# Kernel tuning notes

Measured on AMD Instinct MI355X. Metric: run time of the kernel, lower is better.

The kernel has to match this reference:

```python
import jax, jax.numpy as jnp
import numpy as np


def _refl_conv(x, w, b, pad, stride):
    # ReflectionPad2d(pad) followed by Conv2d(stride=stride), NCHW / OIHW layouts.
    x = jnp.pad(x, ((0, 0), (0, 0), (pad, pad), (pad, pad)), mode='reflect')
    y = jax.lax.conv_general_dilated(
        x, w, window_strides=(stride, stride), padding='VALID',
        dimension_numbers=('NCHW', 'OIHW', 'NCHW'))
    return y + b[None, :, None, None]


def setup_inputs() -> dict:
    key = jax.random.key(0)
    ks = jax.random.split(key, 16)
    B, C, H, W = 8, 128, 64, 64
    IH, IW = 4 * H, 4 * W
    g = 0.02  # init gain ('normal' init in source)
    f32 = jnp.float32
    return {
        'feature_in': jax.random.normal(ks[0], (B, C, H, W), f32),
        'imgs': jax.random.uniform(ks[1], (B, 3, IH, IW), dtype=f32),
        'masks': jax.random.uniform(ks[2], (B, 1, IH, IW), dtype=f32),
        # Gate conv stack params (torch OIHW layout), biases zero per init_weights
        'gw1': g * jax.random.normal(ks[3], (32, 4, 7, 7), f32),
        'gb1': jnp.zeros((32,), f32),
        'gw2': g * jax.random.normal(ks[4], (64, 32, 5, 5), f32),
        'gb2': jnp.zeros((64,), f32),
        'gw3': g * jax.random.normal(ks[5], (128, 64, 5, 5), f32),
        'gb3': jnp.zeros((128,), f32),
        'gw4': g * jax.random.normal(ks[6], (256, 128, 3, 3), f32),
        'gb4': jnp.zeros((256,), f32),
        'gw5': g * jax.random.normal(ks[7], (1, 256, 3, 3), f32),
        'gb5': jnp.zeros((1,), f32),
        # combiner: Conv2d(2C -> C, 1x1)
        'cw': g * jax.random.normal(ks[8], (C, 2 * C, 1, 1), f32),
        'cb': jnp.zeros((C,), f32),
    }


def reference(feature_in, imgs, masks, gw1, gb1, gw2, gb2, gw3, gb3,
              gw4, gb4, gw5, gb5, cw, cb):
    PI = 3.1415926
    # ---- Gate ----
    x = jnp.concatenate([imgs, masks], axis=1)          # [B,4,4H,4W]
    s = jax.nn.relu(_refl_conv(x, gw1, gb1, 3, 1))
    s = jax.nn.relu(_refl_conv(s, gw2, gb2, 2, 2))
    s = jax.nn.relu(_refl_conv(s, gw3, gb3, 2, 1))
    s = jax.nn.relu(_refl_conv(s, gw4, gb4, 1, 2))
    s = jax.nn.relu(_refl_conv(s, gw5, gb5, 1, 1))      # [B,1,H,W]
    s = jnp.tan(PI * (jnp.tanh(s) - 0.5))
    B, C, H, W = feature_in.shape
    P = H * W
    gate = s.reshape(B, P, 1, 1)                        # row-major pixel order
    # ---- Att (patch_size=1: kernels are per-pixel feature vectors) ----
    K = feature_in.reshape(B, C, P).transpose(0, 2, 1) + 1e-7   # [B,P,C]
    Kn = K / jnp.sqrt(jnp.sum(K * K, axis=-1, keepdims=True))
    # attention_scores = conv2d(feature_map, K_norm) == cosine-like similarity
    scores = jnp.einsum('bpc,bcyx->bpyx', Kn, feature_in) + gate  # [B,P,H,W]
    A = jax.nn.softmax(scores, axis=1)
    # conv_transpose2d with 1x1 kernels == weighted sum of (unnormalized) kernels
    att = jnp.einsum('bpyx,bpc->bcyx', A, K)            # [B,C,H,W]
    # ---- combiner (1x1 conv on concat) ----
    cat = jnp.concatenate([att, feature_in], axis=1)    # [B,2C,H,W]
    out = jnp.einsum('oc,bcyx->boyx', cw[:, :, 0, 0], cat) + cb[None, :, None, None]
    return out
```

## Files before the change

### kernel.cpp

```cpp
#include <hip/hip_runtime.h>
#include <hip/hip_bf16.h>
#include <hip/hip_fp16.h>
#include <math.h>


#define PI_F 3.1415926f

typedef __attribute__((ext_vector_type(8))) short short8;
typedef __attribute__((ext_vector_type(4))) float f32x4;
typedef _Float16 half8 __attribute__((ext_vector_type(8)));
typedef __attribute__((ext_vector_type(4))) unsigned short u16x4;
typedef unsigned short ushort_t;

__device__ __forceinline__ ushort_t f2bf(float x) {
    unsigned u = __float_as_uint(x);
    unsigned r = (u + 0x7FFFu + ((u >> 16) & 1u)) >> 16;
    return (ushort_t)r;
}
__device__ __forceinline__ void split16(float x, ushort_t& h, ushort_t& l) {
    __half hh = __float2half(x);
    h = __half_as_ushort(hh);
    l = __half_as_ushort(__float2half(x - __half2float(hh)));
}
__device__ __forceinline__ ushort_t f2h(float x) {
    return __half_as_ushort(__float2half(x));
}
__device__ __forceinline__ int swz(int r, int c) {
    return ((c ^ r ^ (r >> 2)) & 3) << 3;
}

__global__ __launch_bounds__(256) void transform_w_k(
    const float* __restrict__ w, ushort_t* __restrict__ Wh, ushort_t* __restrict__ Wl,
    int Cout, int Cin, int KK)
{
    int idx = blockIdx.x * 256 + threadIdx.x;
    int N = Cout * Cin * KK;
    if (idx >= N) return;
    int oc = idx / (Cin * KK);
    int rem = idx - oc * (Cin * KK);
    int ic = rem / KK;
    int t = rem - ic * KK;
    float v = w[idx];
    long dst = ((long)t * Cout + oc) * Cin + ic;
    split16(v, Wh[dst], Wl[dst]);
}

__global__ __launch_bounds__(256) void transform_w1_k(
    const float* __restrict__ w, ushort_t* __restrict__ Wh, ushort_t* __restrict__ Wl)
{
    int idx = blockIdx.x * 256 + threadIdx.x;
    if (idx >= 7 * 32 * 32) return;
    int ky = idx / 1024;
    int rem = idx - ky * 1024;
    int oc = rem >> 5;
    int k = rem & 31;
    float v = 0.f;
    if (k < 28) {
        int kx = k >> 2, ic = k & 3;
        v = w[((oc * 4 + ic) * 7 + ky) * 7 + kx];
    }
    split16(v, Wh[idx], Wl[idx]);
}

__global__ __launch_bounds__(256) void prep_in_k(
    const float* __restrict__ imgs, const float* __restrict__ masks,
    ushort_t* __restrict__ Xh)
{
    const int iy = blockIdx.x, b = blockIdx.y;
    int sy = iy - 3; if (sy < 0) sy = -sy; if (sy >= 256) sy = 510 - sy;
    const int rb = sy << 8;
    const float* i0 = imgs + (long)b * 3 * 65536;
    const float* mk = masks + (long)b * 65536;
    for (int x = threadIdx.x; x < 262; x += 256) {
        int sx = x - 3; if (sx < 0) sx = -sx; if (sx >= 256) sx = 510 - sx;
        u16x4 hv;
        hv[0] = f2h(i0[rb + sx]);
        hv[1] = f2h(i0[65536 + rb + sx]);
        hv[2] = f2h(i0[131072 + rb + sx]);
        hv[3] = f2h(mk[rb + sx]);
        long o = ((long)(b * 262 + iy) * 262 + x) * 4;
        *(u16x4*)&Xh[o] = hv;
    }
}

__global__ __launch_bounds__(256) void conv1_mfma_k(
    const ushort_t* __restrict__ Xinh,
    const ushort_t* __restrict__ W1h, const ushort_t* __restrict__ W1l,
    const float* __restrict__ bias, ushort_t* __restrict__ Oh)
{
    const int tid = threadIdx.x, lane = tid & 63, wid = tid >> 6;
    const int wm = wid & 1, wn = wid >> 1, l15 = lane & 15, quad = lane >> 4;
    const int ox0 = blockIdx.x * 64;
    const int oy = blockIdx.y, b = blockIdx.z;
    f32x4 acc[2];
    acc[0] = (f32x4){0.f, 0.f, 0.f, 0.f};
    acc[1] = (f32x4){0.f, 0.f, 0.f, 0.f};
#pragma unroll
    for (int ky = 0; ky < 7; ++ky) {
        long wo = (long)(ky * 32 + wm * 16 + l15) * 32 + quad * 8;
        half8 Ah = *(const half8*)&W1h[wo];
        half8 Al = *(const half8*)&W1l[wo];
        long xrow = ((long)(b * 262 + oy + ky) * 262 + ox0) * 4;
#pragma unroll
        for (int ni = 0; ni < 2; ++ni) {
            long xo = xrow + (wn * 32 + ni * 16 + l15) * 4 + quad * 8;
            half8 Bh = *(const half8*)&Xinh[xo];
            acc[ni] = __builtin_amdgcn_mfma_f32_16x16x32_f16(Ah, Bh, acc[ni], 0, 0, 0);
            acc[ni] = __builtin_amdgcn_mfma_f32_16x16x32_f16(Al, Bh, acc[ni], 0, 0, 0);
        }
    }
    const int ocf = wm * 16 + quad * 4;
    float4 bv = *(const float4*)&bias[ocf];
#pragma unroll
    for (int ni = 0; ni < 2; ++ni) {
        int n = ox0 + wn * 32 + ni * 16 + l15;
        u16x4 hv;
        hv[0] = f2h(fmaxf(acc[ni][0] + bv.x, 0.f));
        hv[1] = f2h(fmaxf(acc[ni][1] + bv.y, 0.f));
        hv[2] = f2h(fmaxf(acc[ni][2] + bv.z, 0.f));
        hv[3] = f2h(fmaxf(acc[ni][3] + bv.w, 0.f));
        long o = ((long)(b * 260 + oy + 2) * 260 + n + 2) * 32 + ocf;
        *(u16x4*)&Oh[o] = hv;
    }
}

__global__ __launch_bounds__(256) void pad_cl_k(
    ushort_t* __restrict__ Xh, int Hp, int Wp, int PAD, int C, int H, int W)
{
    const int iy = blockIdx.x, b = blockIdx.y;
    int t = iy - PAD; if (t < 0) t = -t; if (t >= H) t = 2 * H - 2 - t;
    const int iys = t + PAD;
    const long rowd = ((long)(b * Hp + iy) * Wp) * C;
    const long rows = ((long)(b * Hp + iys) * Wp) * C;
    const int nch = Wp * (C >> 3);
    for (int idx = threadIdx.x; idx < nch; idx += 256) {
        int x = idx / (C >> 3);
        int cg = (idx - x * (C >> 3)) << 3;
        int t2 = x - PAD; if (t2 < 0) t2 = -t2; if (t2 >= W) t2 = 2 * W - 2 - t2;
        int xs = t2 + PAD;
        if (xs == x && iys == iy) continue;
        *(int4*)&Xh[rowd + (long)x * C + cg] = *(const int4*)&Xh[rows + (long)xs * C + cg];
    }
}

template<int K, int S, int CIN, int CSTG, int MT, int NPX, bool WRITE_CL>
__global__ __launch_bounds__(256, 2) void conv_mfma_k(
    const ushort_t* __restrict__ Xh,
    const ushort_t* __restrict__ Wh, const ushort_t* __restrict__ Wl,
    const float* __restrict__ bias,
    int Hp, int Wp, int CoutT,
    ushort_t* __restrict__ Oh, int Hpn, int Wpn, int NP,
    float* __restrict__ Ofp)
{
    constexpr int WS = (NPX - 1) * S + K;
    constexpr int WS2 = (WS + 1) / 2;
    constexpr int MF = MT / 32;
    constexpr int NF = NPX / 32;
    __shared__ ushort_t Bsh[WS * CSTG];
    __shared__ ushort_t Ash[K * MT * CSTG];
    __shared__ ushort_t Asl[K * MT * CSTG];
    const int tid = threadIdx.x, lane = tid & 63, wid = tid >> 6;
    const int wm = wid & 1, wn = wid >> 1, l15 = lane & 15, quad = lane >> 4;
    const int bx = blockIdx.x, oy = blockIdx.y;
    const int NOC = CoutT / MT;
    const int ocg = blockIdx.z % NOC, b = blockIdx.z / NOC;
    const int ox0 = bx * NPX;

    f32x4 acc[MF][NF];
#pragma unroll
    for (int mi = 0; mi < MF; ++mi)
#pragma unroll
        for (int ni = 0; ni < NF; ++ni) acc[mi][ni] = (f32x4){0.f, 0.f, 0.f, 0.f};

#pragma unroll
    for (int ky = 0; ky < K; ++ky) {
        const long rowoff = ((long)(b * Hp + oy * S + ky) * Wp + ox0 * S) * CIN;
        for (int cs = 0; cs < CIN; cs += CSTG) {
            __syncthreads();
            constexpr int NCH = WS * CSTG / 8;
#pragma unroll
            for (int it = 0; it < (NCH + 255) / 256; ++it) {
                int flat = tid + it * 256;
                if (flat < NCH) {
                    int e0 = flat * 8;
                    int x = e0 / CSTG;
                    int cpos = (e0 - x * CSTG) >> 3;
                    int xs = (S == 1) ? x : ((x >> 1) + (x & 1) * WS2);
                    *(int4*)&Bsh[xs * CSTG + swz(xs, cpos)] =
                        *(const int4*)&Xh[rowoff + (long)x * CIN + cs + cpos * 8];
                }
            }
            constexpr int NW = K * MT * CSTG / 8;
#pragma unroll
            for (int it = 0; it < (NW + 255) / 256; ++it) {
                int flat = tid + it * 256;
                if (flat < NW) {
                    int e0 = flat * 8;
                    int kx = e0 / (MT * CSTG);
                    int rem = e0 - kx * MT * CSTG;
                    int oc = rem / CSTG;
                    int cpos = (rem - oc * CSTG) >> 3;
                    int arow = kx * MT + oc;
                    int dst = arow * CSTG + swz(arow, cpos);
                    long src = ((long)((ky * K + kx) * CoutT + ocg * MT + oc)) * CIN + cs + cpos * 8;
                    *(int4*)&Ash[dst] = *(const int4*)&Wh[src];
                    *(int4*)&Asl[dst] = *(const int4*)&Wl[src];
                }
            }
            __syncthreads();
#pragma unroll
            for (int kx = 0; kx < K; ++kx) {
                half8 Ah[MF], Al[MF], Bh[NF];
#pragma unroll
                for (int mi = 0; mi < MF; ++mi) {
                    int arow = kx * MT + wm * (MT / 2) + mi * 16 + l15;
                    int ao = arow * CSTG + swz(arow, quad);
                    Ah[mi] = *(const half8*)&Ash[ao];
                    Al[mi] = *(const half8*)&Asl[ao];
                }
#pragma unroll
                for (int ni = 0; ni < NF; ++ni) {
                    int m = wn * (NPX / 2) + ni * 16 + l15;
                    int xs = (S == 1) ? (m + kx) : (m + (kx >> 1) + (kx & 1) * WS2);
                    Bh[ni] = *(const half8*)&Bsh[xs * CSTG + swz(xs, quad)];
                }
#pragma unroll
                for (int mi = 0; mi < MF; ++mi)
#pragma unroll
                    for (int ni = 0; ni < NF; ++ni) {
                        acc[mi][ni] = __builtin_amdgcn_mfma_f32_16x16x32_f16(Ah[mi], Bh[ni], acc[mi][ni], 0, 0, 0);
                        acc[mi][ni] = __builtin_amdgcn_mfma_f32_16x16x32_f16(Al[mi], Bh[ni], acc[mi][ni], 0, 0, 0);
                    }
            }
        }
    }
#pragma unroll
    for (int ni = 0; ni < NF; ++ni) {
        const int n = ox0 + wn * (NPX / 2) + ni * 16 + l15;
#pragma unroll
        for (int mi = 0; mi < MF; ++mi) {
            const int ocf = ocg * MT + wm * (MT / 2) + mi * 16 + quad * 4;
            float4 bv = *(const float4*)&bias[ocf];
            float v0 = fmaxf(acc[mi][ni][0] + bv.x, 0.f);
            float v1 = fmaxf(acc[mi][ni][1] + bv.y, 0.f);
            float v2 = fmaxf(acc[mi][ni][2] + bv.z, 0.f);
            float v3 = fmaxf(acc[mi][ni][3] + bv.w, 0.f);
            if (WRITE_CL) {
                long o = ((long)(b * Hpn + oy + NP) * Wpn + n + NP) * CoutT + ocf;
                u16x4 hv;
                hv[0] = f2h(v0); hv[1] = f2h(v1); hv[2] = f2h(v2); hv[3] = f2h(v3);
                *(u16x4*)&Oh[o] = hv;
            } else {
                long o = ((long)(b * CoutT + ocf) << 12) + (oy << 6) + n;
                Ofp[o] = v0;
                Ofp[o + 4096] = v1;
                Ofp[o + 8192] = v2;
                Ofp[o + 12288] = v3;
            }
        }
    }
}

__global__ __launch_bounds__(256) void conv5_gate_k(
    const float* __restrict__ s4, const float* __restrict__ w,
    const float* __restrict__ bias, float* __restrict__ gate)
{
    const int tid = threadIdx.x;
    const int lane = tid & 63, g = tid >> 6;
    const int oy = blockIdx.x, b = blockIdx.y;
    int ixo[3], iyo[3];
#pragma unroll
    for (int k = 0; k < 3; ++k) {
        int ix = lane + k - 1; if (ix < 0) ix = -ix; if (ix >= 64) ix = 126 - ix;
        int iy = oy + k - 1; if (iy < 0) iy = -iy; if (iy >= 64) iy = 126 - iy;
        ixo[k] = ix; iyo[k] = iy << 6;
    }
    float part = 0.f;
    const float* inb = s4 + ((long)b * 256 + g * 64) * 4096;
    const float* wg = w + g * 64 * 9;
    for (int ic = 0; ic < 64; ++ic) {
        const float* inc = inb + ic * 4096;
        const float* wc = wg + ic * 9;
#pragma unroll
        for (int ky = 0; ky < 3; ++ky)
#pragma unroll
            for (int kx = 0; kx < 3; ++kx)
                part = fmaf(wc[ky * 3 + kx], inc[iyo[ky] + ixo[kx]], part);
    }
    __shared__ float red[4][64];
    red[g][lane] = part;
    __syncthreads();
    if (tid < 64) {
        float s = bias[0] + red[0][tid] + red[1][tid] + red[2][tid] + red[3][tid];
        s = fmaxf(s, 0.f);
        gate[(b << 12) + (oy << 6) + tid] = tanf(PI_F * (tanhf(s) - 0.5f));
    }
}

__global__ __launch_bounds__(256) void invn_k(const float* __restrict__ F, float* __restrict__ invn)
{
    const int p = blockIdx.x * 256 + threadIdx.x;
    const int b = blockIdx.y;
    const float* Fb = F + (long)b * 524288;
    float ss = 0.f;
#pragma unroll 8
    for (int c = 0; c < 128; ++c) {
        float v = Fb[c * 4096 + p] + 1e-7f;
        ss = fmaf(v, v, ss);
    }
    invn[(b << 12) + p] = 1.0f / sqrtf(ss);
}

__global__ __launch_bounds__(256) void prep_bf16_k(
    const float* __restrict__ F, ushort_t* __restrict__ Fo16, ushort_t* __restrict__ Ft16)
{
    __shared__ float Ls[128][65];
    const int tid = threadIdx.x;
    const int lane = tid & 63, wv = tid >> 6;
    const int p0 = blockIdx.x * 64, b = blockIdx.y;
#pragma unroll 8
    for (int cc = 0; cc < 32; ++cc) {
        int c = wv * 32 + cc;
        long idx = ((long)b * 128 + c) * 4096 + p0 + lane;
        float v = F[idx];
        Fo16[idx] = f2bf(v);
        Ls[c][lane] = v;
    }
    __syncthreads();
#pragma unroll 8
    for (int i = 0; i < 32; ++i) {
        int flat = tid + 256 * i;
        int c = flat & 127, pl_ = flat >> 7;
        Ft16[((long)b * 4096 + p0 + pl_) * 128 + c] = f2bf(Ls[c][pl_]);
    }
}

__global__ __launch_bounds__(256, 4) void flash_attn_k(
    const ushort_t* __restrict__ Ft16, const ushort_t* __restrict__ Fo16,
    const float* __restrict__ invn, const float* __restrict__ gate,
    float* __restrict__ Opart, float* __restrict__ lpart)
{
    __shared__ float redS[64][4];
    __shared__ ushort_t Es[2][64][72];
    __shared__ ushort_t Qs[16 * 64 * 8];
    const int tid = threadIdx.x, lane = tid & 63, w = tid >> 6;
    const int l15 = lane & 15, quad = lane >> 4;
    const int q0 = blockIdx.x * 64;
    const int ks = blockIdx.y, b = blockIdx.z;
    const int bp = b << 12;
    const ushort_t* Ftb = Ft16 + (long)b * 4096 * 128;
    const ushort_t* Fob = Fo16 + (long)b * 128 * 4096;

#pragma unroll
    for (int s = tid; s < 1024; s += 256) {
        int f = s >> 6, ls = s & 63;
        int ni = f >> 2, cs = f & 3;
        int q = q0 + ni * 16 + (ls & 15);
        int c = cs * 32 + (ls >> 4) * 8;
        *(short8*)&Qs[s * 8] = *(const short8*)&Ftb[(long)q * 128 + c];
    }

    f32x4 O[2][4];
#pragma unroll
    for (int mi = 0; mi < 2; ++mi)
#pragma unroll
        for (int ni = 0; ni < 4; ++ni) O[mi][ni] = (f32x4){0.f, 0.f, 0.f, 0.f};
    float l_acc[4] = {0.f, 0.f, 0.f, 0.f};

    __syncthreads();

    const int p_beg = ks * 1024;
    int buf = 0;
    for (int p0 = p_beg; p0 < p_beg + 1024; p0 += 64, buf ^= 1) {
        f32x4 Sa[4];
#pragma unroll
        for (int ni = 0; ni < 4; ++ni) Sa[ni] = (f32x4){0.f, 0.f, 0.f, 0.f};
#pragma unroll
        for (int cs = 0; cs < 4; ++cs) {
            short8 Ap = *(const short8*)&Ftb[(long)(p0 + w * 16 + l15) * 128 + cs * 32 + quad * 8];
#pragma unroll
            for (int ni = 0; ni < 4; ++ni) {
                short8 Bqf = *(const short8*)&Qs[((ni * 4 + cs) * 64 + lane) * 8];
                Sa[ni] = __builtin_amdgcn_mfma_f32_16x16x32_bf16(Ap, Bqf, Sa[ni], 0, 0, 0);
            }
        }
        float4 iv = *(const float4*)&invn[bp + p0 + w * 16 + quad * 4];
        float4 gt = *(const float4*)&gate[bp + p0 + w * 16 + quad * 4];
#pragma unroll
        for (int ni = 0; ni < 4; ++ni) {
            float e0 = __expf(fmaf(Sa[ni][0], iv.x, gt.x));
            float e1 = __expf(fmaf(Sa[ni][1], iv.y, gt.y));
            float e2 = __expf(fmaf(Sa[ni][2], iv.z, gt.z));
            float e3 = __expf(fmaf(Sa[ni][3], iv.w, gt.w));
            union { u16x4 v; __hip_bfloat162 h[2]; } u;
            u.h[0] = __float22bfloat162_rn(make_float2(e0, e1));
            u.h[1] = __float22bfloat162_rn(make_float2(e2, e3));
            *(u16x4*)&Es[buf][ni * 16 + l15][w * 16 + quad * 4] = u.v;
            l_acc[ni] += (e0 + e1) + (e2 + e3);
        }
        __syncthreads();
#pragma unroll
        for (int ksub = 0; ksub < 2; ++ksub) {
            short8 Ac[2], Be[4];
#pragma unroll
            for (int mi = 0; mi < 2; ++mi)
                Ac[mi] = *(const short8*)&Fob[(long)(w * 32 + mi * 16 + l15) * 4096 + p0 + ksub * 32 + quad * 8];
#pragma unroll
            for (int ni = 0; ni < 4; ++ni)
                Be[ni] = *(const short8*)&Es[buf][ni * 16 + l15][ksub * 32 + quad * 8];
#pragma unroll
            for (int mi = 0; mi < 2; ++mi)
#pragma unroll
                for (int ni = 0; ni < 4; ++ni)
                    O[mi][ni] = __builtin_amdgcn_mfma_f32_16x16x32_bf16(Ac[mi], Be[ni], O[mi][ni], 0, 0, 0);
        }
    }
#pragma unroll
    for (int ni = 0; ni < 4; ++ni) {
        float lt = l_acc[ni];
        lt += __shfl_xor(lt, 16);
        lt += __shfl_xor(lt, 32);
        if (quad == 0) redS[ni * 16 + l15][w] = lt;
    }
    __syncthreads();
    if (w == 0 && quad == 0) {
#pragma unroll
        for (int ni = 0; ni < 4; ++ni) {
            int q = q0 + ni * 16 + l15;
            float4 rs = *(const float4*)&redS[ni * 16 + l15][0];
            lpart[(ks * 8 + b) * 4096 + q] = (rs.x + rs.y) + (rs.z + rs.w);
        }
    }
    float* Ob = Opart + (long)(ks * 8 + b) * 524288;
#pragma unroll
    for (int mi = 0; mi < 2; ++mi)
#pragma unroll
        for (int ni = 0; ni < 4; ++ni) {
            int c = w * 32 + mi * 16 + quad * 4;
            int q = q0 + ni * 16 + l15;
#pragma unroll
            for (int r = 0; r < 4; ++r)
                Ob[((long)(c + r) << 12) + q] = O[mi][ni][r];
        }
}

__global__ __launch_bounds__(256) void combiner_k(
    const float* __restrict__ Opart, const float* __restrict__ lpart,
    const float* __restrict__ F, const float* __restrict__ cw,
    const float* __restrict__ cb, float* __restrict__ out)
{
    const int tid = threadIdx.x;
    const int q = blockIdx.x * 256 + tid;
    const int o0 = blockIdx.y << 4;
    const int b = blockIdx.z;
    float lsum = 0.f;
#pragma unroll
    for (int ks = 0; ks < 4; ++ks) lsum += lpart[(ks * 8 + b) * 4096 + q];
    float il = 1.0f / lsum;
    const float* Fb = F + (long)b * 524288 + q;
    float acc[16];
#pragma unroll
    for (int j = 0; j < 16; ++j) acc[j] = cb[o0 + j];
    for (int c = 0; c < 128; ++c) {
        float a = 0.f;
#pragma unroll
        for (int ks = 0; ks < 4; ++ks)
            a += Opart[(long)(ks * 8 + b) * 524288 + (long)c * 4096 + q];
        a *= il;
        float f = Fb[(long)c * 4096];
#pragma unroll
        for (int j = 0; j < 16; ++j) {
            acc[j] = fmaf(cw[(o0 + j) * 256 + c], a, acc[j]);
            acc[j] = fmaf(cw[(o0 + j) * 256 + 128 + c], f, acc[j]);
        }
    }
#pragma unroll
    for (int j = 0; j < 16; ++j)
        out[((long)(b * 128 + o0 + j) << 12) + q] = acc[j];
}

extern "C" void kernel_launch(void* const* d_in, const int* in_sizes, int n_in,
                              void* d_out, int out_size, void* d_ws, size_t ws_size,
                              hipStream_t stream)
{
    const float* F     = (const float*)d_in[0];
    const float* imgs  = (const float*)d_in[1];
    const float* masks = (const float*)d_in[2];
    const float* gw1 = (const float*)d_in[3];  const float* gb1 = (const float*)d_in[4];
    const float* gw2 = (const float*)d_in[5];  const float* gb2 = (const float*)d_in[6];
    const float* gw3 = (const float*)d_in[7];  const float* gb3 = (const float*)d_in[8];
    const float* gw4 = (const float*)d_in[9];  const float* gb4 = (const float*)d_in[10];
    const float* gw5 = (const float*)d_in[11]; const float* gb5 = (const float*)d_in[12];
    const float* cw  = (const float*)d_in[13]; const float* cb  = (const float*)d_in[14];
    float* out = (float*)d_out;

    float* W = (float*)d_ws;
    ushort_t* Xcl2h = (ushort_t*)(W);
    ushort_t* Xcl4h = (ushort_t*)(W);
    float*    Opart = W;
    float*    lpart = W + 16777216;
    ushort_t* Xcl3h = (ushort_t*)(W + 17305600);
    ushort_t* Fo16  = (ushort_t*)(W + 17305600);
    float*    s4   = W + 26226688;
    ushort_t* Ft16 = (ushort_t*)(W + 30420992);
    ushort_t* W2h = (ushort_t*)(W + 34615296);
    ushort_t* W2l = (ushort_t*)(W + 34640896);
    ushort_t* W3h = (ushort_t*)(W + 34666496);
    ushort_t* W3l = (ushort_t*)(W + 34768896);
    ushort_t* W4h = (ushort_t*)(W + 34871296);
    ushort_t* W4l = (ushort_t*)(W + 35018752);
    float* gate = W + 35166208;
    float* invn = W + 35198976;
    ushort_t* Xinh = (ushort_t*)(W + 35231744);
    ushort_t* W1h  = (ushort_t*)(W + 37428416);
    ushort_t* W1l  = (ushort_t*)(W + 37432000);

    transform_w_k<<<dim3(200),  256, 0, stream>>>(gw2, W2h, W2l, 64, 32, 25);
    transform_w_k<<<dim3(800),  256, 0, stream>>>(gw3, W3h, W3l, 128, 64, 25);
    transform_w_k<<<dim3(1152), 256, 0, stream>>>(gw4, W4h, W4l, 256, 128, 9);
    transform_w1_k<<<dim3(28), 256, 0, stream>>>(gw1, W1h, W1l);
    prep_in_k<<<dim3(262, 8), 256, 0, stream>>>(imgs, masks, Xinh);

    conv1_mfma_k<<<dim3(4, 256, 8), 256, 0, stream>>>(Xinh, W1h, W1l, gb1, Xcl2h);
    pad_cl_k<<<dim3(260, 8), 256, 0, stream>>>(Xcl2h, 260, 260, 2, 32, 256, 256);
    conv_mfma_k<5, 2, 32, 32, 64, 128, true><<<dim3(1, 128, 8), 256, 0, stream>>>(
        Xcl2h, W2h, W2l, gb2, 260, 260, 64, Xcl3h, 132, 132, 2, nullptr);
    pad_cl_k<<<dim3(132, 8), 256, 0, stream>>>(Xcl3h, 132, 132, 2, 64, 128, 128);
    conv_mfma_k<5, 1, 64, 32, 64, 128, true><<<dim3(1, 128, 16), 256, 0, stream>>>(
        Xcl3h, W3h, W3l, gb3, 132, 132, 128, Xcl4h, 130, 130, 1, nullptr);
    pad_cl_k<<<dim3(130, 8), 256, 0, stream>>>(Xcl4h, 130, 130, 1, 128, 128, 128);
    conv_mfma_k<3, 2, 128, 32, 128, 64, false><<<dim3(1, 64, 16), 256, 0, stream>>>(
        Xcl4h, W4h, W4l, gb4, 130, 130, 256, nullptr, 0, 0, 0, s4);
    conv5_gate_k<<<dim3(64, 8), 256, 0, stream>>>(s4, gw5, gb5, gate);

    invn_k<<<dim3(16, 8), 256, 0, stream>>>(F, invn);
    prep_bf16_k<<<dim3(64, 8), 256, 0, stream>>>(F, Fo16, Ft16);
    flash_attn_k<<<dim3(64, 4, 8), 256, 0, stream>>>(Ft16, Fo16, invn, gate, Opart, lpart);
    combiner_k<<<dim3(16, 8, 8), 256, 0, stream>>>(Opart, lpart, F, cw, cb, out);
}
```

Measured before the change: 629.7 us.

## Software-pipeline flash attention loop and swizzle E tile layout in LDS

Restructures the attention loop so the score MFMAs and exponentials for the next key tile run in the same iteration as the PV MFMAs on the previous tile, with a prologue and epilogue and one barrier per iteration. The E tile in shared memory moves to a fragment-major layout, so each lane reads its B operand as one contiguous short8 rather than from padded rows. The Fo operand loads are issued early in the iteration. The aim is to overlap memory latency, exp work and matrix math and to cut LDS bank conflicts, at the cost of more live registers, which may reduce occupancy under launch_bounds(256,4).

```diff
diff --git a/kernel.cpp b/kernel.cpp
--- a/kernel.cpp
+++ b/kernel.cpp
@@ -341,7 +341,7 @@
     float* __restrict__ Opart, float* __restrict__ lpart)
 {
     __shared__ float redS[64][4];
-    __shared__ ushort_t Es[2][64][72];
+    __shared__ ushort_t Es[2][8 * 64 * 8];
     __shared__ ushort_t Qs[16 * 64 * 8];
     const int tid = threadIdx.x, lane = tid & 63, w = tid >> 6;
     const int l15 = lane & 15, quad = lane >> 4;
@@ -367,11 +367,18 @@
         for (int ni = 0; ni < 4; ++ni) O[mi][ni] = (f32x4){0.f, 0.f, 0.f, 0.f};
     float l_acc[4] = {0.f, 0.f, 0.f, 0.f};
 
+    const int fw = w >> 1;
+    const int Lw = l15 + 16 * ((w & 1) * 2 + (quad >> 1));
+    const int offw = (quad & 1) * 4;
+
     __syncthreads();
 
     const int p_beg = ks * 1024;
-    int buf = 0;
-    for (int p0 = p_beg; p0 < p_beg + 1024; p0 += 64, buf ^= 1) {
+
+    {
+        const int p0 = p_beg;
+        float4 iv = *(const float4*)&invn[bp + p0 + w * 16 + quad * 4];
+        float4 gt = *(const float4*)&gate[bp + p0 + w * 16 + quad * 4];
         f32x4 Sa[4];
 #pragma unroll
         for (int ni = 0; ni < 4; ++ni) Sa[ni] = (f32x4){0.f, 0.f, 0.f, 0.f};
@@ -384,8 +391,6 @@
                 Sa[ni] = __builtin_amdgcn_mfma_f32_16x16x32_bf16(Ap, Bqf, Sa[ni], 0, 0, 0);
             }
         }
-        float4 iv = *(const float4*)&invn[bp + p0 + w * 16 + quad * 4];
-        float4 gt = *(const float4*)&gate[bp + p0 + w * 16 + quad * 4];
 #pragma unroll
         for (int ni = 0; ni < 4; ++ni) {
             float e0 = __expf(fmaf(Sa[ni][0], iv.x, gt.x));
@@ -395,24 +400,79 @@
             union { u16x4 v; __hip_bfloat162 h[2]; } u;
             u.h[0] = __float22bfloat162_rn(make_float2(e0, e1));
             u.h[1] = __float22bfloat162_rn(make_float2(e2, e3));
-            *(u16x4*)&Es[buf][ni * 16 + l15][w * 16 + quad * 4] = u.v;
+            *(u16x4*)&Es[0][((ni * 2 + fw) * 64 + Lw) * 8 + offw] = u.v;
             l_acc[ni] += (e0 + e1) + (e2 + e3);
         }
+    }
+    __syncthreads();
+
+    int buf = 0;
+    for (int t = 1; t < 16; ++t) {
+        const int p0 = p_beg + t * 64;
+        const int p0p = p0 - 64;
+        short8 Ac[2][2];
+#pragma unroll
+        for (int ksub = 0; ksub < 2; ++ksub)
+#pragma unroll
+            for (int mi = 0; mi < 2; ++mi)
+                Ac[ksub][mi] = *(const short8*)&Fob[(long)(w * 32 + mi * 16 + l15) * 4096 + p0p + ksub * 32 + quad * 8];
+        float4 iv = *(const float4*)&invn[bp + p0 + w * 16 + quad * 4];
+        float4 gt = *(const float4*)&gate[bp + p0 + w * 16 + quad * 4];
+        f32x4 Sa[4];
+#pragma unroll
+        for (int ni = 0; ni < 4; ++ni) Sa[ni] = (f32x4){0.f, 0.f, 0.f, 0.f};
+#pragma unroll
+        for (int cs = 0; cs < 4; ++cs) {
+            short8 Ap = *(const short8*)&Ftb[(long)(p0 + w * 16 + l15) * 128 + cs * 32 + quad * 8];
+#pragma unroll
+            for (int ni = 0; ni < 4; ++ni) {
+                short8 Bqf = *(const short8*)&Qs[((ni * 4 + cs) * 64 + lane) * 8];
+                Sa[ni] = __builtin_amdgcn_mfma_f32_16x16x32_bf16(Ap, Bqf, Sa[ni], 0, 0, 0);
+            }
+        }
+#pragma unroll
+        for (int ksub = 0; ksub < 2; ++ksub) {
+            short8 Be[4];
+#pragma unroll
+            for (int ni = 0; ni < 4; ++ni)
+                Be[ni] = *(const short8*)&Es[buf][((ni * 2 + ksub) * 64 + lane) * 8];
+#pragma unroll
+            for (int mi = 0; mi < 2; ++mi)
+#pragma unroll
+                for (int ni = 0; ni < 4; ++ni)
+                    O[mi][ni] = __builtin_amdgcn_mfma_f32_16x16x32_bf16(Ac[ksub][mi], Be[ni], O[mi][ni], 0, 0, 0);
+        }
+#pragma unroll
+        for (int ni = 0; ni < 4; ++ni) {
+            float e0 = __expf(fmaf(Sa[ni][0], iv.x, gt.x));
+            float e1 = __expf(fmaf(Sa[ni][1], iv.y, gt.y));
+            float e2 = __expf(fmaf(Sa[ni][2], iv.z, gt.z));
+            float e3 = __expf(fmaf(Sa[ni][3], iv.w, gt.w));
+            union { u16x4 v; __hip_bfloat162 h[2]; } u;
+            u.h[0] = __float22bfloat162_rn(make_float2(e0, e1));
+            u.h[1] = __float22bfloat162_rn(make_float2(e2, e3));
+            *(u16x4*)&Es[buf ^ 1][((ni * 2 + fw) * 64 + Lw) * 8 + offw] = u.v;
+            l_acc[ni] += (e0 + e1) + (e2 + e3);
+        }
         __syncthreads();
+        buf ^= 1;
+    }
+    {
+        const int p0p = p_beg + 15 * 64;
 #pragma unroll
         for (int ksub = 0; ksub < 2; ++ksub) {
-            short8 Ac[2], Be[4];
+            short8 Ac2[2], Be[4];
 #pragma unroll
             for (int mi = 0; mi < 2; ++mi)
-                Ac[mi] = *(const short8*)&Fob[(long)(w * 32 + mi * 16 + l15) * 4096 + p0 + ksub * 32 + quad * 8];
+                Ac2[mi] = *(const short8*)&Fob[(long)(w * 32 + mi * 16 + l15) * 4096 + p0p + ksub * 32 + quad * 8];
 #pragma unroll
             for (int ni = 0; ni < 4; ++ni)
-                Be[ni] = *(const short8*)&Es[buf][ni * 16 + l15][ksub * 32 + quad * 8];
+                Be[ni] = *(const short8*)&Es[buf][((ni * 2 + ksub) * 64 + lane) * 8];
 #pragma unroll
             for (int mi = 0; mi < 2; ++mi)
 #pragma unroll
                 for (int ni = 0; ni < 4; ++ni)
-                    O[mi][ni] = __builtin_amdgcn_mfma_f32_16x16x32_bf16(Ac[mi], Be[ni], O[mi][ni], 0, 0, 0);
+                    O[mi][ni] = __builtin_amdgcn_mfma_f32_16x16x32_bf16(Ac2[mi], Be[ni], O[mi][ni], 0, 0, 0);
         }
     }
 #pragma unroll
```

Measured after the change: 630.1 us. No clear change (+0.1%).
